# Kernel optimization log

Hardware: AMD Instinct MI355X
Metric: run time of the kernel (lower is better)

## Reference

```python
import jax, jax.numpy as jnp
import numpy as np
import math

NUM_HEADS = 8
KEY_SIZE = 512
EMBED_DIM = 256
BN_EPS = 1e-5


def batchnorm2d_train(x, w, b):
    # x: [B, H, N, hd]; channel axis = 1 (heads). Training-mode batch stats
    # over (B, N, hd), biased variance, as in torch BatchNorm2d forward.
    mean = jnp.mean(x, axis=(0, 2, 3), keepdims=True)
    var = jnp.mean((x - mean) ** 2, axis=(0, 2, 3), keepdims=True)
    xn = (x - mean) * jax.lax.rsqrt(var + BN_EPS)
    return xn * w[None, :, None, None] + b[None, :, None, None]


def l2_normalize(x, axis, eps=1e-12):
    # matches F.normalize(p=2): x / max(||x||, eps)
    n = jnp.sqrt(jnp.sum(x * x, axis=axis, keepdims=True))
    return x / jnp.maximum(n, eps)


def sparsemax(z, axis):
    # Euclidean projection onto the simplex along `axis` (Martins & Astudillo).
    K = z.shape[axis]
    z = z - jnp.max(z, axis=axis, keepdims=True)  # shift-invariant, for stability
    zs = jnp.flip(jnp.sort(z, axis=axis), axis=axis)  # descending sort
    rng_shape = [1] * z.ndim
    rng_shape[axis] = K
    rng = jnp.arange(1, K + 1, dtype=z.dtype).reshape(rng_shape)
    css = jnp.cumsum(zs, axis=axis)
    support = (1.0 + rng * zs) > css
    k_z = jnp.sum(support.astype(jnp.int32), axis=axis, keepdims=True)  # support size >= 1
    tau_sum = jnp.take_along_axis(css, k_z - 1, axis=axis)
    tau = (tau_sum - 1.0) / k_z.astype(z.dtype)
    return jnp.maximum(z - tau, 0.0)


def setup_inputs() -> dict:
    key = jax.random.key(0)
    k1, k2, k3 = jax.random.split(key, 3)
    B, N, C = 8, 1024, EMBED_DIM
    lim = 1.0 / math.sqrt(C)  # torch Linear default init range
    x = jax.random.normal(k1, (B, N, C), dtype=jnp.float32)
    qw = jax.random.uniform(k2, (KEY_SIZE, C), jnp.float32, -lim, lim)
    kw = jax.random.uniform(k3, (KEY_SIZE, C), jnp.float32, -lim, lim)
    bn_weight = jnp.ones((NUM_HEADS,), jnp.float32)
    bn_bias = jnp.zeros((NUM_HEADS,), jnp.float32)
    return {"x": x, "qw": qw, "kw": kw, "bn_weight": bn_weight, "bn_bias": bn_bias}


def reference(x, qw, kw, bn_weight, bn_bias):
    B, N, C = x.shape
    H = NUM_HEADS
    hd = KEY_SIZE // H
    q = jnp.einsum('bnc,kc->bnk', x, qw)  # [B,N,key_size]
    k = jnp.einsum('bnc,kc->bnk', x, kw)
    Q = q.reshape(B, N, H, hd).transpose(0, 2, 1, 3)  # [B,H,N,hd]
    K = k.reshape(B, N, H, hd).transpose(0, 2, 1, 3)
    Q = batchnorm2d_train(Q, bn_weight, bn_bias)
    K = batchnorm2d_train(K, bn_weight, bn_bias)
    Q = l2_normalize(Q, axis=3)
    K = l2_normalize(K, axis=3)
    scores = jnp.einsum('bhnd,bhmd->bhnm', Q, K) / math.sqrt(C)  # scale by sqrt(embeded_dim)
    scores = scores.transpose(0, 2, 1, 3).reshape(B, N, H * N)  # [B,N,H*N]
    # dropout is identity in eval mode
    return sparsemax(scores, axis=1)
```

## Files before the change

### kernel.cpp

```cpp
#include <hip/hip_runtime.h>
#include <math.h>

#define S_STAT 0
#define S_Q    32
#define S_K    (32 + 4194304)
#define S_PL   (32 + 8388608)
#define PLSZ   4194304

typedef unsigned short ushort;
typedef unsigned int uint;
typedef __attribute__((ext_vector_type(8))) short short8;
typedef __attribute__((ext_vector_type(16))) float floatx16;
typedef __attribute__((ext_vector_type(2))) float f32x2;

__device__ __forceinline__ float wave_sum(float v) {
#pragma unroll
    for (int m = 1; m < 64; m <<= 1) v += __shfl_xor(v, m);
    return v;
}

__device__ __forceinline__ ushort f2bf(float f) {
    uint u = __float_as_uint(f);
    uint r = (u + 0x7fffu + ((u >> 16) & 1u)) >> 16;
    return (ushort)r;
}

__global__ __launch_bounds__(64) void k0_zero(float* __restrict__ ws) {
    if (threadIdx.x < 32) ws[S_STAT + threadIdx.x] = 0.0f;
}

__global__ __launch_bounds__(256) void k_pre(const float* __restrict__ x,
                                             const float* __restrict__ qw,
                                             const float* __restrict__ kw,
                                             float* __restrict__ ws) {
    ushort* base = (ushort*)(ws + S_PL) + 4 * PLSZ;
    ushort* XH = base;
    ushort* XL = XH + 2097152;
    ushort* WH = XL + 2097152;
    ushort* WL = WH + 262144;
    const int bid = blockIdx.x;
    const int tid = threadIdx.x;
    const float* __restrict__ src;
    ushort *dh, *dl;
    int idx4;
    if (bid < 2048)      { src = x;  dh = XH;           dl = XL;           idx4 = bid * 256 + tid; }
    else if (bid < 2176) { src = qw; dh = WH;           dl = WL;           idx4 = (bid - 2048) * 256 + tid; }
    else                 { src = kw; dh = WH + 131072;  dl = WL + 131072;  idx4 = (bid - 2176) * 256 + tid; }
    const float4 v = *(const float4*)(src + (size_t)idx4 * 4);
    ushort4 hv, lv;
    {
        hv.x = f2bf(v.x); lv.x = f2bf(v.x - __uint_as_float(((uint)hv.x) << 16));
        hv.y = f2bf(v.y); lv.y = f2bf(v.y - __uint_as_float(((uint)hv.y) << 16));
        hv.z = f2bf(v.z); lv.z = f2bf(v.z - __uint_as_float(((uint)hv.z) << 16));
        hv.w = f2bf(v.w); lv.w = f2bf(v.w - __uint_as_float(((uint)hv.w) << 16));
    }
    *(ushort4*)(dh + (size_t)idx4 * 4) = hv;
    *(ushort4*)(dl + (size_t)idx4 * 4) = lv;
}

__global__ __launch_bounds__(256, 2) void k1_mfma(float* __restrict__ ws) {
    const ushort* base = (const ushort*)(ws + S_PL) + 4 * PLSZ;
    const ushort* __restrict__ XH = base;
    const ushort* __restrict__ XL = XH + 2097152;
    const ushort* __restrict__ WH = XL + 2097152;
    const ushort* __restrict__ WL = WH + 262144;
    const int t = threadIdx.x;
    const int l = t & 63;
    const int w = t >> 6;
    const int rw = w & 1, cw = w >> 1;
    const int row0 = blockIdx.x * 128 + rw * 64;
    const int col0 = blockIdx.y * 128 + cw * 64;
    const int lane31 = l & 31;
    const int kb8 = (l >> 5) * 8;

    floatx16 acc[2][2] = {};
#pragma unroll 4
    for (int kc = 0; kc < 256; kc += 16) {
        short8 ah[2], al[2], bh[2], bl[2];
#pragma unroll
        for (int rt = 0; rt < 2; ++rt) {
            const size_t o = (size_t)(row0 + rt * 32 + lane31) * 256 + kc + kb8;
            ah[rt] = *(const short8*)(XH + o);
            al[rt] = *(const short8*)(XL + o);
        }
#pragma unroll
        for (int ct = 0; ct < 2; ++ct) {
            const size_t o = (size_t)(col0 + ct * 32 + lane31) * 256 + kc + kb8;
            bh[ct] = *(const short8*)(WH + o);
            bl[ct] = *(const short8*)(WL + o);
        }
#pragma unroll
        for (int rt = 0; rt < 2; ++rt)
#pragma unroll
            for (int ct = 0; ct < 2; ++ct) {
                acc[rt][ct] = __builtin_amdgcn_mfma_f32_32x32x16_bf16(ah[rt], bh[ct], acc[rt][ct], 0, 0, 0);
                acc[rt][ct] = __builtin_amdgcn_mfma_f32_32x32x16_bf16(al[rt], bh[ct], acc[rt][ct], 0, 0, 0);
                acc[rt][ct] = __builtin_amdgcn_mfma_f32_32x32x16_bf16(ah[rt], bl[ct], acc[rt][ct], 0, 0, 0);
            }
    }

    const bool is_q = (col0 < 512);
    float* __restrict__ outp = ws + (is_q ? S_Q : S_K);
    const int cbase = col0 & 511;
    const int rsub = 4 * (l >> 5);
    float s1 = 0.f, s2 = 0.f;
#pragma unroll
    for (int rt = 0; rt < 2; ++rt)
#pragma unroll
        for (int ct = 0; ct < 2; ++ct)
#pragma unroll
            for (int e = 0; e < 16; ++e) {
                const int r = row0 + rt * 32 + rsub + (e & 3) + 8 * (e >> 2);
                const int c = cbase + ct * 32 + lane31;
                const float v = acc[rt][ct][e];
                outp[(size_t)r * 512 + c] = v;
                s1 += v; s2 += v * v;
            }
    s1 = wave_sum(s1);
    s2 = wave_sum(s2);
    if (l == 0) {
        const int head = (cbase >> 6) & 7;
        const int sb = (is_q ? 0 : 16) + head;
        atomicAdd(ws + S_STAT + sb, s1);
        atomicAdd(ws + S_STAT + sb + 8, s2);
    }
}

__global__ __launch_bounds__(256) void k3_norm(const float* __restrict__ bnw,
                                               const float* __restrict__ bnb,
                                               float* __restrict__ ws) {
    const int t = threadIdx.x;
    const int w = t >> 6, l = t & 63;
    const int nb = blockIdx.x;
    const int bh = blockIdx.y;
    const int b = bh >> 3, h = bh & 7;
    const int z = blockIdx.z;
    const float* __restrict__ in = ws + (z ? S_K : S_Q);
    const float* st = ws + S_STAT + (z ? 16 : 0);
    ushort* __restrict__ PH = (ushort*)(ws + S_PL) + (z ? 2 * PLSZ : 0) + (size_t)bh * 65536;
    ushort* __restrict__ PL = PH + PLSZ;
    const float inv_m = 1.0f / 524288.0f;
    const float mean  = st[h] * inv_m;
    const float var   = st[8 + h] * inv_m - mean * mean;
    const float alpha = rsqrtf(var + 1e-5f) * bnw[h];
    const float beta  = bnb[h] - mean * alpha;
    const float scale = z ? 0.0625f : 1.0f;

#pragma unroll 1
    for (int i = 0; i < 16; ++i) {
        const int n = nb * 64 + w * 16 + i;
        float v = in[(size_t)(b * 1024 + n) * 512 + h * 64 + l];
        v = fmaf(v, alpha, beta);
        float ss = wave_sum(v * v);
        v = v / fmaxf(sqrtf(ss), 1e-12f) * scale;
        ushort h16 = f2bf(v);
        float hif = __uint_as_float(((uint)h16) << 16);
        ushort l16 = f2bf(v - hif);
        const int idx = n * 64 + l;
        PH[idx] = h16;
        PL[idx] = l16;
    }
}

__global__ __launch_bounds__(256, 2) void k4_attn(const float* __restrict__ ws,
                                                  float* __restrict__ out) {
    __shared__ float part[4][4][32];
    const int t = threadIdx.x;
    const int l = t & 63;
    const int w = t >> 6;
    const int bid = blockIdx.x;
    const int bh = bid & 63;
    const int mt = bid >> 6;
    const int b = bh >> 3, h = bh & 7;
    const int m0 = mt * 32;
    const ushort* __restrict__ QH = (const ushort*)(ws + S_PL);
    const ushort* __restrict__ QL = QH + PLSZ;
    const ushort* __restrict__ KH = QH + 2 * PLSZ;
    const ushort* __restrict__ KL = QH + 3 * PLSZ;

    const int row = l & 31;
    const int kb8 = l >> 5;

    short8 kf[2][4];
#pragma unroll
    for (int ks = 0; ks < 4; ++ks) {
        const size_t off = (size_t)(bh * 1024 + m0 + row) * 64 + ks * 16 + kb8 * 8;
        kf[0][ks] = *(const short8*)(KH + off);
        kf[1][ks] = *(const short8*)(KL + off);
    }

    floatx16 acc[8] = {};

#pragma unroll
    for (int r = 0; r < 8; ++r) {
        const size_t qoff = (size_t)(bh * 1024 + w * 256 + r * 32 + row) * 64 + kb8 * 8;
#pragma unroll
        for (int ks = 0; ks < 4; ++ks) {
            short8 ah = *(const short8*)(QH + qoff + ks * 16);
            short8 al = *(const short8*)(QL + qoff + ks * 16);
            acc[r] = __builtin_amdgcn_mfma_f32_32x32x16_bf16(ah, kf[0][ks], acc[r], 0, 0, 0);
            acc[r] = __builtin_amdgcn_mfma_f32_32x32x16_bf16(al, kf[0][ks], acc[r], 0, 0, 0);
            acc[r] = __builtin_amdgcn_mfma_f32_32x32x16_bf16(ah, kf[1][ks], acc[r], 0, 0, 0);
        }
    }

    const int col = row;

    {
        f32x2 sv = {0.f, 0.f};
#pragma unroll
        for (int r = 0; r < 8; ++r)
#pragma unroll
            for (int p = 0; p < 8; ++p) {
                f32x2 z2 = { acc[r][2 * p], acc[r][2 * p + 1] };
                sv += z2;
            }
        float vsuml = sv.x + sv.y;
        vsuml += __shfl_xor(vsuml, 32);
        if (l < 32) part[2][w][col] = vsuml;
    }
    __syncthreads();
    const float vsum = part[2][0][col] + part[2][1][col]
                     + part[2][2][col] + part[2][3][col];

    float tcur = (vsum - 1.0f) * (1.0f / 1024.0f);
    float tprev = tcur, sprev = 0.f;
#pragma unroll 1
    for (int it = 0; it < 6; ++it) {
        f32x2 s2v = {0.f, 0.f};
#pragma unroll
        for (int r = 0; r < 8; ++r) {
            f32x2 sr = {0.f, 0.f};
#pragma unroll
            for (int p = 0; p < 8; ++p) {
                f32x2 z2 = { acc[r][2 * p], acc[r][2 * p + 1] };
                f32x2 d = z2 - tcur;
                d.x = fmaxf(d.x, 0.f);
                d.y = fmaxf(d.y, 0.f);
                sr += d;
            }
            s2v += sr;
        }
        float sl = s2v.x + s2v.y;
        sl += __shfl_xor(sl, 32);
        if (l < 32) part[it & 1][w][col] = sl;
        __syncthreads();
        const float s = part[it & 1][0][col] + part[it & 1][1][col]
                      + part[it & 1][2][col] + part[it & 1][3][col];
        const float g = s - 1.0f;
        float step;
        if (it == 0) {
            step = g * (1.0f / 1024.0f);
        } else {
            const float denom = sprev - s;
            step = (denom > 1e-30f) ? g * (tcur - tprev) / denom : 0.f;
        }
        step = fmaxf(step, 0.f);
        tprev = tcur; sprev = s;
        tcur += step;
    }

    float cntl = 0.f, ssml = 0.f;
#pragma unroll
    for (int r = 0; r < 8; ++r)
#pragma unroll
        for (int e = 0; e < 16; ++e) {
            const float zz = acc[r][e];
            if (zz > tcur) { cntl += 1.f; ssml += zz; }
        }
    cntl += __shfl_xor(cntl, 32);
    ssml += __shfl_xor(ssml, 32);
    if (l < 32) { part[2][w][col] = cntl; part[3][w][col] = ssml; }
    __syncthreads();
    const float cnt  = part[2][0][col] + part[2][1][col] + part[2][2][col] + part[2][3][col];
    const float ssum = part[3][0][col] + part[3][1][col] + part[3][2][col] + part[3][3][col];
    const float tau = (ssum - 1.0f) / cnt;

    float* __restrict__ ob = out + (size_t)b * 1024 * 8192 + h * 1024 + m0 + col;
    const int nbase = w * 256 + 4 * kb8;
#pragma unroll
    for (int r = 0; r < 8; ++r)
#pragma unroll
        for (int e = 0; e < 16; ++e) {
            const int n = nbase + r * 32 + (e & 3) + 8 * (e >> 2);
            __builtin_nontemporal_store(fmaxf(acc[r][e] - tau, 0.f),
                                        ob + (size_t)n * 8192);
        }
}

extern "C" void kernel_launch(void* const* d_in, const int* in_sizes, int n_in,
                              void* d_out, int out_size, void* d_ws, size_t ws_size,
                              hipStream_t stream) {
    (void)in_sizes; (void)n_in; (void)out_size; (void)ws_size;
    const float* x   = (const float*)d_in[0];
    const float* qw  = (const float*)d_in[1];
    const float* kw  = (const float*)d_in[2];
    const float* bnw = (const float*)d_in[3];
    const float* bnb = (const float*)d_in[4];
    float* ws  = (float*)d_ws;
    float* out = (float*)d_out;

    hipLaunchKernelGGL(k0_zero, dim3(1), dim3(64), 0, stream, ws);
    hipLaunchKernelGGL(k_pre, dim3(2304), dim3(256), 0, stream, x, qw, kw, ws);
    hipLaunchKernelGGL(k1_mfma, dim3(64, 8), dim3(256), 0, stream, ws);
    hipLaunchKernelGGL(k3_norm, dim3(16, 64, 2), dim3(256), 0, stream, bnw, bnb, ws);
    hipLaunchKernelGGL(k4_attn, dim3(2048), dim3(256), 0, stream, ws, out);
}
```

Measured before the change: 476.9 us.

## Split attention into tau pass and recompute pass with coalesced row-major stores

The fused attention kernel is split in two. The first kernel computes only the per-column sparsemax threshold tau and writes it to the workspace. The second recomputes the score tiles per query-row block, stages them in shared memory transposed, and writes contiguous float4 rows to the output instead of scattered stride-8192 scalar stores. This trades a second full MFMA score computation and an extra launch for much better write coalescing on the 256MB output.

Result: slower. 506.8 us (+6.3%).

```diff
diff --git a/kernel.cpp b/kernel.cpp
--- a/kernel.cpp
+++ b/kernel.cpp
@@ -12,6 +12,7 @@
 typedef __attribute__((ext_vector_type(8))) short short8;
 typedef __attribute__((ext_vector_type(16))) float floatx16;
 typedef __attribute__((ext_vector_type(2))) float f32x2;
+typedef __attribute__((ext_vector_type(4))) float f32x4;
 
 __device__ __forceinline__ float wave_sum(float v) {
 #pragma unroll
@@ -162,8 +163,7 @@
     }
 }
 
-__global__ __launch_bounds__(256, 2) void k4_attn(const float* __restrict__ ws,
-                                                  float* __restrict__ out) {
+__global__ __launch_bounds__(256, 2) void k4a_tau(float* __restrict__ ws) {
     __shared__ float part[4][4][32];
     const int t = threadIdx.x;
     const int l = t & 63;
@@ -171,7 +171,6 @@
     const int bid = blockIdx.x;
     const int bh = bid & 63;
     const int mt = bid >> 6;
-    const int b = bh >> 3, h = bh & 7;
     const int m0 = mt * 32;
     const ushort* __restrict__ QH = (const ushort*)(ws + S_PL);
     const ushort* __restrict__ QL = QH + PLSZ;
@@ -276,16 +275,83 @@
     const float ssum = part[3][0][col] + part[3][1][col] + part[3][2][col] + part[3][3][col];
     const float tau = (ssum - 1.0f) / cnt;
 
-    float* __restrict__ ob = out + (size_t)b * 1024 * 8192 + h * 1024 + m0 + col;
-    const int nbase = w * 256 + 4 * kb8;
-#pragma unroll
-    for (int r = 0; r < 8; ++r)
-#pragma unroll
-        for (int e = 0; e < 16; ++e) {
-            const int n = nbase + r * 32 + (e & 3) + 8 * (e >> 2);
-            __builtin_nontemporal_store(fmaxf(acc[r][e] - tau, 0.f),
-                                        ob + (size_t)n * 8192);
-        }
+    if (t < 32) ws[S_Q + bh * 1024 + m0 + t] = tau;
+}
+
+__global__ __launch_bounds__(256, 2) void k4b_store(const float* __restrict__ ws,
+                                                    float* __restrict__ out) {
+    __shared__ float st[32][512];
+    const int t = threadIdx.x;
+    const int l = t & 63;
+    const int w = t >> 6;
+    const int bid = blockIdx.x;
+    const int bh = bid & 63;
+    const int nt = bid >> 6;
+    const int b = bh >> 3, h = bh & 7;
+    const int n0 = nt * 32;
+    const ushort* __restrict__ QH = (const ushort*)(ws + S_PL);
+    const ushort* __restrict__ QL = QH + PLSZ;
+    const ushort* __restrict__ KH = QH + 2 * PLSZ;
+    const ushort* __restrict__ KL = QH + 3 * PLSZ;
+    const float* __restrict__ tauBuf = ws + S_Q + bh * 1024;
+
+    const int row = l & 31;
+    const int kb8 = l >> 5;
+
+    short8 qf[2][4];
+#pragma unroll
+    for (int ks = 0; ks < 4; ++ks) {
+        const size_t off = (size_t)(bh * 1024 + n0 + row) * 64 + ks * 16 + kb8 * 8;
+        qf[0][ks] = *(const short8*)(QH + off);
+        qf[1][ks] = *(const short8*)(QL + off);
+    }
+
+    float* __restrict__ obase = out + (size_t)b * 1024 * 8192 + h * 1024;
+
+#pragma unroll 1
+    for (int rnd = 0; rnd < 2; ++rnd) {
+        const int mchunk = rnd * 512;
+
+        floatx16 acc[4] = {};
+#pragma unroll
+        for (int mt = 0; mt < 4; ++mt) {
+            const int ml = mchunk + w * 128 + mt * 32;
+#pragma unroll
+            for (int ks = 0; ks < 4; ++ks) {
+                const size_t off = (size_t)(bh * 1024 + ml + row) * 64 + ks * 16 + kb8 * 8;
+                short8 bhf = *(const short8*)(KH + off);
+                short8 blf = *(const short8*)(KL + off);
+                acc[mt] = __builtin_amdgcn_mfma_f32_32x32x16_bf16(qf[0][ks], bhf, acc[mt], 0, 0, 0);
+                acc[mt] = __builtin_amdgcn_mfma_f32_32x32x16_bf16(qf[1][ks], bhf, acc[mt], 0, 0, 0);
+                acc[mt] = __builtin_amdgcn_mfma_f32_32x32x16_bf16(qf[0][ks], blf, acc[mt], 0, 0, 0);
+            }
+        }
+
+        __syncthreads();
+#pragma unroll
+        for (int mt = 0; mt < 4; ++mt) {
+            const int mloc = w * 128 + mt * 32 + row;
+            const float taum = tauBuf[mchunk + mloc];
+#pragma unroll
+            for (int e = 0; e < 16; ++e) {
+                const int n = (e & 3) + 8 * (e >> 2) + 4 * kb8;
+                st[n][mloc] = fmaxf(acc[mt][e] - taum, 0.f);
+            }
+        }
+        __syncthreads();
+
+#pragma unroll
+        for (int j = 0; j < 8; ++j) {
+            const int n = w * 8 + j;
+            float* __restrict__ orow = obase + (size_t)(n0 + n) * 8192 + mchunk;
+#pragma unroll
+            for (int i = 0; i < 2; ++i) {
+                const int moff = i * 256 + l * 4;
+                const f32x4 v = *(const f32x4*)&st[n][moff];
+                __builtin_nontemporal_store(v, (f32x4*)(orow + moff));
+            }
+        }
+    }
 }
 
 extern "C" void kernel_launch(void* const* d_in, const int* in_sizes, int n_in,
@@ -304,5 +370,6 @@
     hipLaunchKernelGGL(k_pre, dim3(2304), dim3(256), 0, stream, x, qw, kw, ws);
     hipLaunchKernelGGL(k1_mfma, dim3(64, 8), dim3(256), 0, stream, ws);
     hipLaunchKernelGGL(k3_norm, dim3(16, 64, 2), dim3(256), 0, stream, bnw, bnb, ws);
-    hipLaunchKernelGGL(k4_attn, dim3(2048), dim3(256), 0, stream, ws, out);
-}
+    hipLaunchKernelGGL(k4a_tau, dim3(2048), dim3(256), 0, stream, ws);
+    hipLaunchKernelGGL(k4b_store, dim3(2048), dim3(256), 0, stream, ws, out);
+}
```
